# Kernel tuning notes

Measured on AMD Instinct MI355X. Metric: run time of the kernel, lower is better.

The kernel has to match this reference:

```python
import jax, jax.numpy as jnp
import numpy as np

N, C, H, W = 4, 256, 64, 64
K, G, PAD, STRIDE, DIL = 3, 8, 1, 1, 1
GC = C // G      # channels per group
P = K * K        # sampling points per group
HIN, WIN = H + 2 * PAD, W + 2 * PAD
BN_EPS = 1e-5
LN_EPS = 1e-5


def setup_inputs():
    key = jax.random.key(0)
    ks = jax.random.split(key, 8)
    f32 = jnp.float32
    return {
        "x": jax.random.normal(ks[0], (N, C, H, W), dtype=f32),
        "w_in": jax.random.normal(ks[1], (C, C), dtype=f32) * 0.05,
        "b_in": jnp.zeros((C,), f32),
        "w_dw": jax.random.normal(ks[2], (C, 1, K, K), dtype=f32) * 0.1,
        "b_dw": jnp.zeros((C,), f32),
        "ln_g": jnp.ones((C,), f32), "ln_b": jnp.zeros((C,), f32),
        "w_off": jax.random.normal(ks[3], (C, G * P * 2), dtype=f32) * 0.01,
        "b_off": jax.random.normal(ks[4], (G * P * 2,), dtype=f32) * 0.01,
        "w_mask": jax.random.normal(ks[5], (C, G * P), dtype=f32) * 0.01,
        "b_mask": jnp.zeros((G * P,), f32),
        "w_out": jax.random.normal(ks[6], (C, C), dtype=f32) * 0.05,
        "b_out": jnp.zeros((C,), f32),
        "bn_g": jnp.ones((C,), f32), "bn_b": jnp.zeros((C,), f32),
        "bn_mean": jnp.zeros((C,), f32), "bn_var": jnp.ones((C,), f32),
    }


def _bilinear(img, grid):
    # img: (B, Cc, Hh, Ww); grid: (B, S, P, 2) normalized to [-1,1],
    # matches F.grid_sample(mode='bilinear', padding_mode='zeros', align_corners=False)
    B, Cc, Hh, Ww = img.shape
    gx = (grid[..., 0] + 1.0) * 0.5 * Ww - 0.5
    gy = (grid[..., 1] + 1.0) * 0.5 * Hh - 0.5
    x0 = jnp.floor(gx)
    y0 = jnp.floor(gy)
    wx = gx - x0
    wy = gy - y0
    flat = img.reshape(B, Cc, Hh * Ww)

    def tap(xi, yi, wgt):
        valid = (xi >= 0) & (xi <= Ww - 1) & (yi >= 0) & (yi <= Hh - 1)
        idx = (jnp.clip(yi, 0, Hh - 1) * Ww + jnp.clip(xi, 0, Ww - 1)).astype(jnp.int32)
        v = jax.vmap(lambda im, ix: im[:, ix])(flat, idx)   # (B, Cc, S, P)
        return v * (wgt * valid.astype(img.dtype))[:, None]

    return (tap(x0, y0, (1 - wx) * (1 - wy)) + tap(x0 + 1, y0, wx * (1 - wy))
            + tap(x0, y0 + 1, (1 - wx) * wy) + tap(x0 + 1, y0 + 1, wx * wy))


def _forward(x, w_in, b_in, w_dw, b_dw, ln_g, ln_b, w_off, b_off,
             w_mask, b_mask, w_out, b_out, bn_g, bn_b, bn_mean, bn_var):
    xl = jnp.transpose(x, (0, 2, 3, 1))                      # (N,H,W,C) channels-last
    x_proj = xl @ w_in + b_in                                # input_proj
    # depthwise conv + LayerNorm + GELU feature branch for offset/mask prediction
    dw = jax.lax.conv_general_dilated(
        x, w_dw, (1, 1), ((PAD, PAD), (PAD, PAD)),
        feature_group_count=C, dimension_numbers=("NCHW", "OIHW", "NCHW"))
    dw = jnp.transpose(dw + b_dw[None, :, None, None], (0, 2, 3, 1))
    mu = dw.mean(-1, keepdims=True)
    var = ((dw - mu) ** 2).mean(-1, keepdims=True)
    dw = (dw - mu) * jax.lax.rsqrt(var + LN_EPS) * ln_g + ln_b
    x1 = jax.nn.gelu(dw, approximate=False)
    offset = x1 @ w_off + b_off                              # (N,H,W,G*P*2)
    mask = jax.nn.softmax((x1 @ w_mask + b_mask).reshape(N, H, W, G, P), axis=-1)
    # reference points + dilation kernel grid, normalized to padded input, (x,y) order
    ry = ((DIL * (K - 1)) // 2 + 0.5 + jnp.arange(H, dtype=x.dtype) * STRIDE) / HIN
    rx = ((DIL * (K - 1)) // 2 + 0.5 + jnp.arange(W, dtype=x.dtype) * STRIDE) / WIN
    ref = jnp.stack(jnp.broadcast_arrays(rx[None, :], ry[:, None]), axis=-1)  # (H,W,2)
    px = (jnp.arange(K, dtype=x.dtype) * DIL - (DIL * (K - 1)) // 2) / WIN
    py = (jnp.arange(K, dtype=x.dtype) * DIL - (DIL * (K - 1)) // 2) / HIN
    gx, gy = jnp.meshgrid(px, py, indexing="ij")             # kw-major flattening as in DCNv3
    kgrid = jnp.stack([gx, gy], -1).reshape(P, 2)
    norm = jnp.array([WIN, HIN], dtype=x.dtype)
    loc = (ref[None, :, :, None, None, :] + kgrid[None, None, None, None, :, :]
           + offset.reshape(N, H, W, G, P, 2) / norm)        # (N,H,W,G,P,2), offset_scale=1
    sgrid = 2.0 * loc - 1.0
    # group-split padded value tensor and deformable sampling
    xp = jnp.pad(x_proj, ((0, 0), (PAD, PAD), (PAD, PAD), (0, 0)))
    img = jnp.transpose(xp, (0, 3, 1, 2)).reshape(N * G, GC, HIN, WIN)
    sg = jnp.transpose(sgrid.reshape(N, H * W, G, P, 2), (0, 2, 1, 3, 4)).reshape(N * G, H * W, P, 2)
    sampled = _bilinear(img, sg)                             # (N*G, GC, H*W, P)
    m = jnp.transpose(mask.reshape(N, H * W, G, P), (0, 2, 1, 3)).reshape(N * G, 1, H * W, P)
    agg = (sampled * m).sum(-1)                              # (N*G, GC, H*W)
    y = jnp.transpose(agg.reshape(N, C, H * W), (0, 2, 1)).reshape(N, H, W, C)
    y = y @ w_out + b_out                                    # output_proj
    y = jnp.transpose(y, (0, 3, 1, 2))                       # back to NCHW
    y = (y - bn_mean[None, :, None, None]) * jax.lax.rsqrt(bn_var + BN_EPS)[None, :, None, None]
    y = y * bn_g[None, :, None, None] + bn_b[None, :, None, None]
    return y * jax.nn.sigmoid(y)                             # SiLU (Conv.default_act)


def reference(x, w_in, b_in, w_dw, b_dw, ln_g, ln_b, w_off, b_off,
              w_mask, b_mask, w_out, b_out, bn_g, bn_b, bn_mean, bn_var):
    return _forward(x, w_in, b_in, w_dw, b_dw, ln_g, ln_b, w_off, b_off,
                    w_mask, b_mask, w_out, b_out, bn_g, bn_b, bn_mean, bn_var)
```

## Files before the change

### kernel.cpp

```cpp
#include <hip/hip_runtime.h>
#include <math.h>

#define NB   4
#define CCH  256
#define HH   64
#define WW   64
#define GG   8
#define GCH  32
#define PP   9
#define HIN  66
#define WIN  66
#define HWSZ 4096
#define NPIX 16384

#define X16_ELEMS (NPIX*CCH)
#define XP_ELEMS  (NB*HIN*WIN*CCH)
#define X1_ELEMS  (NPIX*CCH)
#define AGG_ELEMS (NPIX*CCH)
#define WIN16_ELEMS (CCH*CCH)
#define WOUT16_ELEMS (CCH*CCH)
#define WOM16_ELEMS (CCH*216)
#define OFF_ELEMS (NPIX*144)
#define MSK_ELEMS (NPIX*72)

typedef __attribute__((ext_vector_type(8))) short bf16x8;
typedef __attribute__((ext_vector_type(4))) float f32x4;

__device__ __forceinline__ unsigned short f2bf(float f) {
    unsigned int u = __float_as_uint(f);
    unsigned int r = (u + 0x7FFFu + ((u >> 16) & 1u)) >> 16;
    return (unsigned short)r;
}
__device__ __forceinline__ float bf2f(unsigned short s) {
    return __uint_as_float(((unsigned int)s) << 16);
}

#define AK 40

__global__ __launch_bounds__(256) void k_prep(
    const float* __restrict__ x, const float* __restrict__ w_in,
    const float* __restrict__ w_off, const float* __restrict__ w_mask,
    const float* __restrict__ w_out, unsigned short* __restrict__ x16,
    unsigned short* __restrict__ w_in16, unsigned short* __restrict__ wom16,
    unsigned short* __restrict__ w_out16, unsigned short* __restrict__ xp)
{
    const int b = blockIdx.x;
    const int tid = threadIdx.x;
    if (b < 2048) {
        size_t i0 = (size_t)b * 2048 + tid * 4;
#pragma unroll
        for (int h = 0; h < 2; h++) {
            float4 v = *(const float4*)&x[i0 + h * 1024];
            ushort4 o;
            o.x = f2bf(v.x); o.y = f2bf(v.y); o.z = f2bf(v.z); o.w = f2bf(v.w);
            *(ushort4*)&x16[i0 + h * 1024] = o;
        }
    } else if (b < 2096) {
        int gtid = (b - 2048) * 256 + tid;
        for (int i = gtid; i < 186368; i += 12288) {
            if (i < 65536) {
                w_in16[i] = f2bf(w_in[i]);
            } else if (i < 131072) {
                int j = i - 65536;
                w_out16[j] = f2bf(w_out[j]);
            } else {
                int j = i - 131072;
                int r = j / 216, c = j - r * 216;
                float v = (c < 144) ? w_off[r * 144 + c] : w_mask[r * 72 + c - 144];
                wom16[j] = f2bf(v);
            }
        }
    } else {
        int idx = (b - 2096) * 256 + tid;
        int seg = idx >> 6, ln = idx & 63;
        int n = seg / 260, rp = seg % 260;
        int h, w;
        if (rp < 66)       { h = 0;        w = rp; }
        else if (rp < 132) { h = 65;       w = rp - 66; }
        else if (rp < 196) { h = rp - 131; w = 0; }
        else               { h = rp - 195; w = 65; }
        uint2 z = make_uint2(0u, 0u);
        *(uint2*)&xp[(((size_t)n * HIN + h) * WIN + w) * CCH + ln * 4] = z;
    }
}

__global__ __launch_bounds__(256) void k_gemm_in(
    const unsigned short* __restrict__ x16, const unsigned short* __restrict__ w16,
    const float* __restrict__ b_in, unsigned short* __restrict__ xp)
{
    __shared__ short As[128 * AK];
    __shared__ short Ws[64 * AK];

    const int m0  = blockIdx.x * 128;
    const int co0 = blockIdx.y * 64;
    const int tid = threadIdx.x;
    const int n   = m0 >> 12;
    const int hw0 = m0 & 4095;

    const int wave = tid >> 6;
    const int lane = tid & 63;
    const int r16  = lane & 15;
    const int quad = lane >> 4;
    const int mw   = wave * 32;

    const unsigned short* xa = x16 + (size_t)n * CCH * HWSZ + hw0;

    f32x4 acc[2][4];
#pragma unroll
    for (int i = 0; i < 2; i++)
#pragma unroll
        for (int j = 0; j < 4; j++) acc[i][j] = (f32x4){0.f, 0.f, 0.f, 0.f};

    for (int k0 = 0; k0 < CCH; k0 += 32) {
#pragma unroll
        for (int l = 0; l < 4; l++) {
            int idx = tid + l * 256;
            int m = idx & 127, kph = idx >> 7;
            unsigned int u0 = xa[(size_t)(k0 + 4 * kph + 0) * HWSZ + m];
            unsigned int u1 = xa[(size_t)(k0 + 4 * kph + 1) * HWSZ + m];
            unsigned int u2 = xa[(size_t)(k0 + 4 * kph + 2) * HWSZ + m];
            unsigned int u3 = xa[(size_t)(k0 + 4 * kph + 3) * HWSZ + m];
            uint2 pk = make_uint2(u0 | (u1 << 16), u2 | (u3 << 16));
            *(uint2*)&As[m * AK + kph * 4] = pk;
        }
#pragma unroll
        for (int l = 0; l < 2; l++) {
            int idx = tid + l * 256;
            int nn = idx & 63, kph = idx >> 6;
            unsigned int u0 = w16[(size_t)(k0 + 4 * kph + 0) * CCH + co0 + nn];
            unsigned int u1 = w16[(size_t)(k0 + 4 * kph + 1) * CCH + co0 + nn];
            unsigned int u2 = w16[(size_t)(k0 + 4 * kph + 2) * CCH + co0 + nn];
            unsigned int u3 = w16[(size_t)(k0 + 4 * kph + 3) * CCH + co0 + nn];
            uint2 pk = make_uint2(u0 | (u1 << 16), u2 | (u3 << 16));
            *(uint2*)&Ws[nn * AK + kph * 4] = pk;
        }
        __syncthreads();

        bf16x8 a0 = *(const bf16x8*)&As[(mw + r16) * AK + quad * 8];
        bf16x8 a1 = *(const bf16x8*)&As[(mw + 16 + r16) * AK + quad * 8];
#pragma unroll
        for (int nt = 0; nt < 4; nt++) {
            bf16x8 bfr = *(const bf16x8*)&Ws[(nt * 16 + r16) * AK + quad * 8];
            acc[0][nt] = __builtin_amdgcn_mfma_f32_16x16x32_bf16(a0, bfr, acc[0][nt], 0, 0, 0);
            acc[1][nt] = __builtin_amdgcn_mfma_f32_16x16x32_bf16(a1, bfr, acc[1][nt], 0, 0, 0);
        }
        __syncthreads();
    }

#pragma unroll
    for (int nt = 0; nt < 4; nt++) {
        int co = co0 + nt * 16 + r16;
        float bias = b_in[co];
#pragma unroll
        for (int mt = 0; mt < 2; mt++) {
            int mbase = mw + mt * 16 + quad * 4;
#pragma unroll
            for (int r = 0; r < 4; r++) {
                int hw = hw0 + mbase + r;
                int h = hw >> 6, w = hw & 63;
                xp[(((size_t)n * HIN + (h + 1)) * WIN + (w + 1)) * CCH + co] =
                    f2bf(acc[mt][nt][r] + bias);
            }
        }
    }
}

#define SDW_STRIDE 258
__global__ __launch_bounds__(512) void k_dw_ln_gelu(
    const unsigned short* __restrict__ x16, const float* __restrict__ w_dw,
    const float* __restrict__ b_dw, const float* __restrict__ ln_g,
    const float* __restrict__ ln_b, unsigned short* __restrict__ x1)
{
    __shared__ unsigned short sdw[64 * SDW_STRIDE];
    __shared__ float r1s[8][64];
    __shared__ float r2s[8][64];
    __shared__ float mu_s[64];
    __shared__ float rs_s[64];

    const int h = blockIdx.x;
    const int n = blockIdx.y;
    const int tid = threadIdx.x;
    const int wave = tid >> 6;
    const int lane = tid & 63;

    const unsigned short* xn = x16 + (size_t)n * CCH * HWSZ;
    const bool h0ok = (h > 0);
    const bool h2ok = (h < HH - 1);

    float s1 = 0.f, s2 = 0.f;

#pragma unroll 4
    for (int it = 0; it < 32; it++) {
        const int c = it * 8 + wave;
        const unsigned short* xc = xn + (size_t)c * HWSZ + h * WW + lane;
        float v0 = h0ok ? bf2f(xc[-WW]) : 0.f;
        float v1 = bf2f(xc[0]);
        float v2 = h2ok ? bf2f(xc[WW]) : 0.f;

        const float* wk = w_dw + c * 9;
        float acc = b_dw[c];

        float l0 = __shfl_up(v0, 1);  if (lane == 0)  l0 = 0.f;
        float r0 = __shfl_down(v0, 1); if (lane == 63) r0 = 0.f;
        acc += wk[0] * l0 + wk[1] * v0 + wk[2] * r0;

        float l1 = __shfl_up(v1, 1);  if (lane == 0)  l1 = 0.f;
        float r1 = __shfl_down(v1, 1); if (lane == 63) r1 = 0.f;
        acc += wk[3] * l1 + wk[4] * v1 + wk[5] * r1;

        float l2 = __shfl_up(v2, 1);  if (lane == 0)  l2 = 0.f;
        float r2 = __shfl_down(v2, 1); if (lane == 63) r2 = 0.f;
        acc += wk[6] * l2 + wk[7] * v2 + wk[8] * r2;

        s1 += acc;
        s2 += acc * acc;
        sdw[lane * SDW_STRIDE + c] = f2bf(acc);
    }

    r1s[wave][lane] = s1;
    r2s[wave][lane] = s2;
    __syncthreads();

    if (tid < 64) {
        float a1 = 0.f, a2 = 0.f;
#pragma unroll
        for (int q = 0; q < 8; q++) { a1 += r1s[q][tid]; a2 += r2s[q][tid]; }
        float mu = a1 * (1.0f / 256.0f);
        float var = a2 * (1.0f / 256.0f) - mu * mu;
        mu_s[tid] = mu;
        rs_s[tid] = rsqrtf(var + 1e-5f);
    }
    __syncthreads();

    const int c0 = (tid & 63) * 4;
    const int wq = tid >> 6;
    float g4[4], b4[4];
#pragma unroll
    for (int i = 0; i < 4; i++) { g4[i] = ln_g[c0 + i]; b4[i] = ln_b[c0 + i]; }

    unsigned short* x1p = x1 + (((size_t)n * HH + h) * WW) * CCH + c0;
#pragma unroll
    for (int pass = 0; pass < 8; pass++) {
        int w = wq + pass * 8;
        float mu = mu_s[w], rs = rs_s[w];
        const unsigned short* row = &sdw[w * SDW_STRIDE + c0];
        unsigned short tmp[4];
#pragma unroll
        for (int i = 0; i < 4; i++) {
            float v = (bf2f(row[i]) - mu) * rs * g4[i] + b4[i];
            tmp[i] = f2bf(0.5f * v * (1.0f + erff(v * 0.70710678118654752f)));
        }
        ushort4 o; o.x = tmp[0]; o.y = tmp[1]; o.z = tmp[2]; o.w = tmp[3];
        *(ushort4*)&x1p[(size_t)w * CCH] = o;
    }
}

__global__ __launch_bounds__(256) void k_gemm_offmask(
    const unsigned short* __restrict__ x1, const unsigned short* __restrict__ wom16,
    const float* __restrict__ b_off, const float* __restrict__ b_mask,
    float* __restrict__ off, float* __restrict__ msk)
{
    __shared__ short As[128 * AK];
    __shared__ short Ws[64 * AK];

    const int m0  = blockIdx.x * 128;
    const int co0 = blockIdx.y * 64;
    const int tid = threadIdx.x;

    const int wave = tid >> 6;
    const int lane = tid & 63;
    const int r16  = lane & 15;
    const int quad = lane >> 4;
    const int mw   = wave * 32;

    f32x4 acc[2][4];
#pragma unroll
    for (int i = 0; i < 2; i++)
#pragma unroll
        for (int j = 0; j < 4; j++) acc[i][j] = (f32x4){0.f, 0.f, 0.f, 0.f};

    for (int k0 = 0; k0 < CCH; k0 += 32) {
#pragma unroll
        for (int l = 0; l < 2; l++) {
            int idx = tid + l * 256;
            int m = idx >> 2, kq = idx & 3;
            uint4 v = *(const uint4*)&x1[(size_t)(m0 + m) * CCH + k0 + kq * 8];
            *(uint4*)&As[m * AK + kq * 8] = v;
        }
#pragma unroll
        for (int l = 0; l < 2; l++) {
            int idx = tid + l * 256;
            int nn = idx & 63, kph = idx >> 6;
            int col = co0 + nn;
            unsigned int u0 = 0, u1 = 0, u2 = 0, u3 = 0;
            if (col < 216) {
                u0 = wom16[(size_t)(k0 + 4 * kph + 0) * 216 + col];
                u1 = wom16[(size_t)(k0 + 4 * kph + 1) * 216 + col];
                u2 = wom16[(size_t)(k0 + 4 * kph + 2) * 216 + col];
                u3 = wom16[(size_t)(k0 + 4 * kph + 3) * 216 + col];
            }
            uint2 pk = make_uint2(u0 | (u1 << 16), u2 | (u3 << 16));
            *(uint2*)&Ws[nn * AK + kph * 4] = pk;
        }
        __syncthreads();

        bf16x8 a0 = *(const bf16x8*)&As[(mw + r16) * AK + quad * 8];
        bf16x8 a1 = *(const bf16x8*)&As[(mw + 16 + r16) * AK + quad * 8];
#pragma unroll
        for (int nt = 0; nt < 4; nt++) {
            bf16x8 bfr = *(const bf16x8*)&Ws[(nt * 16 + r16) * AK + quad * 8];
            acc[0][nt] = __builtin_amdgcn_mfma_f32_16x16x32_bf16(a0, bfr, acc[0][nt], 0, 0, 0);
            acc[1][nt] = __builtin_amdgcn_mfma_f32_16x16x32_bf16(a1, bfr, acc[1][nt], 0, 0, 0);
        }
        __syncthreads();
    }

#pragma unroll
    for (int nt = 0; nt < 4; nt++) {
        int col = co0 + nt * 16 + r16;
        if (col >= 216) continue;
        float bias = (col < 144) ? b_off[col] : b_mask[col - 144];
#pragma unroll
        for (int mt = 0; mt < 2; mt++) {
            int mbase = m0 + mw + mt * 16 + quad * 4;
#pragma unroll
            for (int r = 0; r < 4; r++) {
                int p = mbase + r;
                float v = acc[mt][nt][r] + bias;
                if (col < 144) off[(size_t)p * 144 + col] = v;
                else           msk[(size_t)p * 72 + col - 144] = v;
            }
        }
    }
}

__device__ __forceinline__ void acc8_tap(float* a, uint4 vv, float wgt) {
    a[0] += wgt * __uint_as_float(vv.x << 16);
    a[1] += wgt * __uint_as_float(vv.x & 0xffff0000u);
    a[2] += wgt * __uint_as_float(vv.y << 16);
    a[3] += wgt * __uint_as_float(vv.y & 0xffff0000u);
    a[4] += wgt * __uint_as_float(vv.z << 16);
    a[5] += wgt * __uint_as_float(vv.z & 0xffff0000u);
    a[6] += wgt * __uint_as_float(vv.w << 16);
    a[7] += wgt * __uint_as_float(vv.w & 0xffff0000u);
}

__global__ __launch_bounds__(256) void k_sample_agg(
    const unsigned short* __restrict__ xp, const float* __restrict__ off,
    const float* __restrict__ msk, unsigned short* __restrict__ agg)
{
    __shared__ float  sm[576];
    __shared__ int2   tco[576];
    __shared__ float4 twt[576];

    const int tid = threadIdx.x;
    const int s0 = blockIdx.x * 8;

    if (tid < 64) {
        const int pix = tid >> 3, g = tid & 7;
        const float* mskp = msk + (size_t)(s0 + pix) * 72 + g * 9;
        float e[9];
        float mx = -1e30f;
#pragma unroll
        for (int p = 0; p < PP; p++) { e[p] = mskp[p]; mx = fmaxf(mx, e[p]); }
        float sum = 0.f;
#pragma unroll
        for (int p = 0; p < PP; p++) { e[p] = __expf(e[p] - mx); sum += e[p]; }
        float rs = 1.0f / sum;
#pragma unroll
        for (int p = 0; p < PP; p++) sm[tid * 9 + p] = e[p] * rs;
    }
    __syncthreads();

    for (int idx = tid; idx < 576; idx += 256) {
        int pix = idx / 72;
        int rem = idx - pix * 72;
        int g = rem / 9;
        int p = rem - g * 9;
        int s = s0 + pix;
        int hw = s & 4095;
        int h = hw >> 6, w = hw & 63;
        const float* offp = off + (size_t)s * 144 + g * 18 + p * 2;
        float ox = offp[0], oy = offp[1];
        int i = p / 3, j = p - i * 3;
        float fx = (float)(w + i) + ox;
        float fy = (float)(h + j) + oy;
        float x0f = floorf(fx), y0f = floorf(fy);
        int x0 = (int)x0f, y0 = (int)y0f;
        float wx = fx - x0f, wy = fy - y0f;
        float m = sm[idx];
        float w00 = (1.f - wx) * (1.f - wy) * m;
        float w10 = wx * (1.f - wy) * m;
        float w01 = (1.f - wx) * wy * m;
        float w11 = wx * wy * m;
        int x1c = x0 + 1, y1c = y0 + 1;
        if (!((x0  >= 0) && (x0  < WIN))) { w00 = 0.f; w01 = 0.f; }
        if (!((x1c >= 0) && (x1c < WIN))) { w10 = 0.f; w11 = 0.f; }
        if (!((y0  >= 0) && (y0  < HIN))) { w00 = 0.f; w10 = 0.f; }
        if (!((y1c >= 0) && (y1c < HIN))) { w01 = 0.f; w11 = 0.f; }
        int cx0 = min(max(x0, 0), WIN - 1), cx1 = min(max(x1c, 0), WIN - 1);
        int cy0 = min(max(y0, 0), HIN - 1), cy1 = min(max(y1c, 0), HIN - 1);
        tco[idx] = make_int2(cx0 | (cx1 << 16), cy0 | (cy1 << 16));
        twt[idx] = make_float4(w00, w10, w01, w11);
    }
    __syncthreads();

    const int pix = tid >> 5;
    const int l5 = tid & 31;
    const int g = l5 >> 2, c8 = l5 & 3;
    const int s = s0 + pix;
    const int n = s >> 12;
    const unsigned short* base = xp + (size_t)n * HIN * WIN * CCH + g * GCH + c8 * 8;
    const int tbase = pix * 72 + g * 9;

    float a[8];
#pragma unroll
    for (int i = 0; i < 8; i++) a[i] = 0.f;

#pragma unroll
    for (int p = 0; p < PP; p++) {
        int2 cc = tco[tbase + p];
        float4 wt = twt[tbase + p];
        int cx0 = cc.x & 0xFFFF, cx1 = cc.x >> 16;
        int cy0 = cc.y & 0xFFFF, cy1 = cc.y >> 16;
        const unsigned short* r0 = base + (size_t)(cy0 * WIN) * CCH;
        const unsigned short* r1 = base + (size_t)(cy1 * WIN) * CCH;
        uint4 v00 = *(const uint4*)&r0[(size_t)cx0 * CCH];
        uint4 v10 = *(const uint4*)&r0[(size_t)cx1 * CCH];
        uint4 v01 = *(const uint4*)&r1[(size_t)cx0 * CCH];
        uint4 v11 = *(const uint4*)&r1[(size_t)cx1 * CCH];
        acc8_tap(a, v00, wt.x);
        acc8_tap(a, v10, wt.y);
        acc8_tap(a, v01, wt.z);
        acc8_tap(a, v11, wt.w);
    }

    uint4 o;
    o.x = (unsigned int)f2bf(a[0]) | ((unsigned int)f2bf(a[1]) << 16);
    o.y = (unsigned int)f2bf(a[2]) | ((unsigned int)f2bf(a[3]) << 16);
    o.z = (unsigned int)f2bf(a[4]) | ((unsigned int)f2bf(a[5]) << 16);
    o.w = (unsigned int)f2bf(a[6]) | ((unsigned int)f2bf(a[7]) << 16);
    *(uint4*)&agg[(size_t)s * CCH + g * GCH + c8 * 8] = o;
}

__global__ __launch_bounds__(256) void k_gemm_out(
    const unsigned short* __restrict__ agg, const unsigned short* __restrict__ w16,
    const float* __restrict__ b_out, const float* __restrict__ bn_g,
    const float* __restrict__ bn_b, const float* __restrict__ bn_mean,
    const float* __restrict__ bn_var, float* __restrict__ out)
{
    __shared__ short As[128 * AK];
    __shared__ short Ws[64 * AK];

    const int m0  = blockIdx.x * 128;
    const int co0 = blockIdx.y * 64;
    const int tid = threadIdx.x;
    const int n   = m0 >> 12;
    const int hw0 = m0 & 4095;

    const int wave = tid >> 6;
    const int lane = tid & 63;
    const int r16  = lane & 15;
    const int quad = lane >> 4;
    const int mw   = wave * 32;

    f32x4 acc[2][4];
#pragma unroll
    for (int i = 0; i < 2; i++)
#pragma unroll
        for (int j = 0; j < 4; j++) acc[i][j] = (f32x4){0.f, 0.f, 0.f, 0.f};

    for (int k0 = 0; k0 < CCH; k0 += 32) {
#pragma unroll
        for (int l = 0; l < 2; l++) {
            int idx = tid + l * 256;
            int m = idx >> 2, kq = idx & 3;
            uint4 v = *(const uint4*)&agg[(size_t)(m0 + m) * CCH + k0 + kq * 8];
            *(uint4*)&As[m * AK + kq * 8] = v;
        }
#pragma unroll
        for (int l = 0; l < 2; l++) {
            int idx = tid + l * 256;
            int nn = idx & 63, kph = idx >> 6;
            unsigned int u0 = w16[(size_t)(k0 + 4 * kph + 0) * CCH + co0 + nn];
            unsigned int u1 = w16[(size_t)(k0 + 4 * kph + 1) * CCH + co0 + nn];
            unsigned int u2 = w16[(size_t)(k0 + 4 * kph + 2) * CCH + co0 + nn];
            unsigned int u3 = w16[(size_t)(k0 + 4 * kph + 3) * CCH + co0 + nn];
            uint2 pk = make_uint2(u0 | (u1 << 16), u2 | (u3 << 16));
            *(uint2*)&Ws[nn * AK + kph * 4] = pk;
        }
        __syncthreads();

        bf16x8 a0 = *(const bf16x8*)&As[(mw + r16) * AK + quad * 8];
        bf16x8 a1 = *(const bf16x8*)&As[(mw + 16 + r16) * AK + quad * 8];
#pragma unroll
        for (int nt = 0; nt < 4; nt++) {
            bf16x8 bfr = *(const bf16x8*)&Ws[(nt * 16 + r16) * AK + quad * 8];
            acc[0][nt] = __builtin_amdgcn_mfma_f32_16x16x32_bf16(a0, bfr, acc[0][nt], 0, 0, 0);
            acc[1][nt] = __builtin_amdgcn_mfma_f32_16x16x32_bf16(a1, bfr, acc[1][nt], 0, 0, 0);
        }
        __syncthreads();
    }

#pragma unroll
    for (int nt = 0; nt < 4; nt++) {
        int co = co0 + nt * 16 + r16;
        float mean = bn_mean[co];
        float rstd = rsqrtf(bn_var[co] + 1e-5f);
        float gg = bn_g[co], bb = bn_b[co], bo = b_out[co];
#pragma unroll
        for (int mt = 0; mt < 2; mt++) {
            int hwb = hw0 + mw + mt * 16 + quad * 4;
            float tmp[4];
#pragma unroll
            for (int r = 0; r < 4; r++) {
                float y = acc[mt][nt][r] + bo;
                float yh = (y - mean) * rstd * gg + bb;
                tmp[r] = yh / (1.0f + __expf(-yh));
            }
            float4 v = make_float4(tmp[0], tmp[1], tmp[2], tmp[3]);
            *(float4*)&out[((size_t)n * CCH + co) * HWSZ + hwb] = v;
        }
    }
}

extern "C" void kernel_launch(void* const* d_in, const int* in_sizes, int n_in,
                              void* d_out, int out_size, void* d_ws, size_t ws_size,
                              hipStream_t stream)
{
    const float* x       = (const float*)d_in[0];
    const float* w_in    = (const float*)d_in[1];
    const float* b_in    = (const float*)d_in[2];
    const float* w_dw    = (const float*)d_in[3];
    const float* b_dw    = (const float*)d_in[4];
    const float* ln_g    = (const float*)d_in[5];
    const float* ln_b    = (const float*)d_in[6];
    const float* w_off   = (const float*)d_in[7];
    const float* b_off   = (const float*)d_in[8];
    const float* w_mask  = (const float*)d_in[9];
    const float* b_mask  = (const float*)d_in[10];
    const float* w_out   = (const float*)d_in[11];
    const float* b_out   = (const float*)d_in[12];
    const float* bn_g    = (const float*)d_in[13];
    const float* bn_b    = (const float*)d_in[14];
    const float* bn_mean = (const float*)d_in[15];
    const float* bn_var  = (const float*)d_in[16];
    float* out = (float*)d_out;

    unsigned short* x16    = (unsigned short*)d_ws;
    unsigned short* xp     = x16 + X16_ELEMS;
    unsigned short* x1     = xp + XP_ELEMS;
    unsigned short* agg    = x1 + X1_ELEMS;
    unsigned short* w_in16 = agg + AGG_ELEMS;
    unsigned short* w_out16= w_in16 + WIN16_ELEMS;
    unsigned short* wom16  = w_out16 + WOUT16_ELEMS;
    float* off = (float*)(wom16 + WOM16_ELEMS);
    float* msk = off + OFF_ELEMS;

    k_prep<<<dim3(2356), 256, 0, stream>>>(x, w_in, w_off, w_mask, w_out,
                                           x16, w_in16, wom16, w_out16, xp);
    k_gemm_in<<<dim3(128, 4), 256, 0, stream>>>(x16, w_in16, b_in, xp);
    k_dw_ln_gelu<<<dim3(64, 4), 512, 0, stream>>>(x16, w_dw, b_dw, ln_g, ln_b, x1);
    k_gemm_offmask<<<dim3(128, 4), 256, 0, stream>>>(x1, wom16, b_off, b_mask, off, msk);
    k_sample_agg<<<dim3(2048), 256, 0, stream>>>(xp, off, msk, agg);
    k_gemm_out<<<dim3(128, 4), 256, 0, stream>>>(agg, w_out16, b_out, bn_g, bn_b, bn_mean, bn_var, out);
}
```

Measured before the change: 198.6 us.

## Fuse prep with depthwise-LN-GELU, merge input and offset GEMMs, drop LDS staging

The bf16 conversion of x now happens inside the depthwise/LayerNorm/GELU kernel, which reads fp32 x directly and also writes an NHWC bf16 copy of x. That kernel is merged with the weight-transpose and padding work into one launch. The input projection and the offset/mask projection GEMMs now share one launch with 1024 blocks. All GEMMs load A fragments and transposed weight fragments straight from global memory, with no shared-memory tiles or barriers. This cuts the launch count from six to four and removes a strided NCHW gather and the LDS round trips. The cost is more redundant global/L2 traffic for the weight fragments, and a dw kernel with more shared memory and only 256 compute blocks.

```diff
diff --git a/kernel.cpp b/kernel.cpp
--- a/kernel.cpp
+++ b/kernel.cpp
@@ -13,15 +13,15 @@
 #define HWSZ 4096
 #define NPIX 16384
 
-#define X16_ELEMS (NPIX*CCH)
-#define XP_ELEMS  (NB*HIN*WIN*CCH)
-#define X1_ELEMS  (NPIX*CCH)
-#define AGG_ELEMS (NPIX*CCH)
-#define WIN16_ELEMS (CCH*CCH)
-#define WOUT16_ELEMS (CCH*CCH)
-#define WOM16_ELEMS (CCH*216)
-#define OFF_ELEMS (NPIX*144)
-#define MSK_ELEMS (NPIX*72)
+#define X16_ELEMS  (NPIX*CCH)
+#define XP_ELEMS   (NB*HIN*WIN*CCH)
+#define X1_ELEMS   (NPIX*CCH)
+#define AGG_ELEMS  (NPIX*CCH)
+#define WINT_ELEMS (CCH*CCH)
+#define WOUTT_ELEMS (CCH*CCH)
+#define WOMT_ELEMS (216*CCH)
+#define OFF_ELEMS  (NPIX*144)
+#define MSK_ELEMS  (NPIX*72)
 
 typedef __attribute__((ext_vector_type(8))) short bf16x8;
 typedef __attribute__((ext_vector_type(4))) float f32x4;
@@ -35,300 +35,238 @@
     return __uint_as_float(((unsigned int)s) << 16);
 }
 
-#define AK 40
-
-__global__ __launch_bounds__(256) void k_prep(
-    const float* __restrict__ x, const float* __restrict__ w_in,
+#define SDW_STRIDE 258
+
+__global__ __launch_bounds__(512) void k_dw_prep(
+    const float* __restrict__ x, const float* __restrict__ w_dw,
+    const float* __restrict__ b_dw, const float* __restrict__ ln_g,
+    const float* __restrict__ ln_b, const float* __restrict__ w_in,
     const float* __restrict__ w_off, const float* __restrict__ w_mask,
-    const float* __restrict__ w_out, unsigned short* __restrict__ x16,
-    unsigned short* __restrict__ w_in16, unsigned short* __restrict__ wom16,
-    unsigned short* __restrict__ w_out16, unsigned short* __restrict__ xp)
+    const float* __restrict__ w_out, unsigned short* __restrict__ x1,
+    unsigned short* __restrict__ x16, unsigned short* __restrict__ win_t,
+    unsigned short* __restrict__ womt, unsigned short* __restrict__ wout_t,
+    unsigned short* __restrict__ xp)
 {
     const int b = blockIdx.x;
     const int tid = threadIdx.x;
-    if (b < 2048) {
-        size_t i0 = (size_t)b * 2048 + tid * 4;
-#pragma unroll
-        for (int h = 0; h < 2; h++) {
-            float4 v = *(const float4*)&x[i0 + h * 1024];
-            ushort4 o;
-            o.x = f2bf(v.x); o.y = f2bf(v.y); o.z = f2bf(v.z); o.w = f2bf(v.w);
-            *(ushort4*)&x16[i0 + h * 1024] = o;
-        }
-    } else if (b < 2096) {
-        int gtid = (b - 2048) * 256 + tid;
-        for (int i = gtid; i < 186368; i += 12288) {
+
+    if (b >= 256) {
+        const int gtid = (b - 256) * 512 + tid;
+        const int STRIDE = 68 * 512;
+        for (int i = gtid; i < 252928; i += STRIDE) {
             if (i < 65536) {
-                w_in16[i] = f2bf(w_in[i]);
+                int n = i & 255, k = i >> 8;
+                win_t[n * 256 + k] = f2bf(w_in[i]);
             } else if (i < 131072) {
                 int j = i - 65536;
-                w_out16[j] = f2bf(w_out[j]);
+                int n = j & 255, k = j >> 8;
+                wout_t[n * 256 + k] = f2bf(w_out[j]);
+            } else if (i < 186368) {
+                int j = i - 131072;
+                int k = j / 216, col = j - k * 216;
+                float v = (col < 144) ? w_off[k * 144 + col]
+                                      : w_mask[k * 72 + col - 144];
+                womt[col * 256 + k] = f2bf(v);
             } else {
-                int j = i - 131072;
-                int r = j / 216, c = j - r * 216;
-                float v = (c < 144) ? w_off[r * 144 + c] : w_mask[r * 72 + c - 144];
-                wom16[j] = f2bf(v);
-            }
-        }
-    } else {
-        int idx = (b - 2096) * 256 + tid;
-        int seg = idx >> 6, ln = idx & 63;
-        int n = seg / 260, rp = seg % 260;
-        int h, w;
-        if (rp < 66)       { h = 0;        w = rp; }
-        else if (rp < 132) { h = 65;       w = rp - 66; }
-        else if (rp < 196) { h = rp - 131; w = 0; }
-        else               { h = rp - 195; w = 65; }
-        uint2 z = make_uint2(0u, 0u);
-        *(uint2*)&xp[(((size_t)n * HIN + h) * WIN + w) * CCH + ln * 4] = z;
-    }
-}
-
-__global__ __launch_bounds__(256) void k_gemm_in(
-    const unsigned short* __restrict__ x16, const unsigned short* __restrict__ w16,
-    const float* __restrict__ b_in, unsigned short* __restrict__ xp)
+                int r = i - 186368;
+                int seg = r >> 6, ln = r & 63;
+                int n = seg / 260, rp = seg % 260;
+                int h, w;
+                if (rp < 66)       { h = 0;        w = rp; }
+                else if (rp < 132) { h = 65;       w = rp - 66; }
+                else if (rp < 196) { h = rp - 131; w = 0; }
+                else               { h = rp - 195; w = 65; }
+                uint2 z = make_uint2(0u, 0u);
+                *(uint2*)&xp[(((size_t)n * HIN + h) * WIN + w) * CCH + ln * 4] = z;
+            }
+        }
+        return;
+    }
+
+    __shared__ unsigned short sdw[64 * SDW_STRIDE];
+    __shared__ unsigned short sxr[64 * SDW_STRIDE];
+    __shared__ float r1s[8][64];
+    __shared__ float r2s[8][64];
+    __shared__ float mu_s[64];
+    __shared__ float rs_s[64];
+
+    const int h = b & 63;
+    const int n = b >> 6;
+    const int wave = tid >> 6;
+    const int lane = tid & 63;
+
+    const float* xn = x + (size_t)n * CCH * HWSZ;
+    const bool h0ok = (h > 0);
+    const bool h2ok = (h < HH - 1);
+
+    float s1 = 0.f, s2 = 0.f;
+
+#pragma unroll 4
+    for (int it = 0; it < 32; it++) {
+        const int c = it * 8 + wave;
+        const float* xc = xn + (size_t)c * HWSZ + h * WW + lane;
+        float v0 = h0ok ? xc[-WW] : 0.f;
+        float v1 = xc[0];
+        float v2 = h2ok ? xc[WW] : 0.f;
+
+        const float* wk = w_dw + c * 9;
+        float acc = b_dw[c];
+
+        float l0 = __shfl_up(v0, 1);   if (lane == 0)  l0 = 0.f;
+        float r0 = __shfl_down(v0, 1); if (lane == 63) r0 = 0.f;
+        acc += wk[0] * l0 + wk[1] * v0 + wk[2] * r0;
+
+        float l1 = __shfl_up(v1, 1);   if (lane == 0)  l1 = 0.f;
+        float r1 = __shfl_down(v1, 1); if (lane == 63) r1 = 0.f;
+        acc += wk[3] * l1 + wk[4] * v1 + wk[5] * r1;
+
+        float l2 = __shfl_up(v2, 1);   if (lane == 0)  l2 = 0.f;
+        float r2 = __shfl_down(v2, 1); if (lane == 63) r2 = 0.f;
+        acc += wk[6] * l2 + wk[7] * v2 + wk[8] * r2;
+
+        s1 += acc;
+        s2 += acc * acc;
+        sdw[lane * SDW_STRIDE + c] = f2bf(acc);
+        sxr[lane * SDW_STRIDE + c] = f2bf(v1);
+    }
+
+    r1s[wave][lane] = s1;
+    r2s[wave][lane] = s2;
+    __syncthreads();
+
+    if (tid < 64) {
+        float a1 = 0.f, a2 = 0.f;
+#pragma unroll
+        for (int q = 0; q < 8; q++) { a1 += r1s[q][tid]; a2 += r2s[q][tid]; }
+        float mu = a1 * (1.0f / 256.0f);
+        float var = a2 * (1.0f / 256.0f) - mu * mu;
+        mu_s[tid] = mu;
+        rs_s[tid] = rsqrtf(var + 1e-5f);
+    }
+    __syncthreads();
+
+    const int c0 = (tid & 63) * 4;
+    const int wq = tid >> 6;
+    float g4[4], b4[4];
+#pragma unroll
+    for (int i = 0; i < 4; i++) { g4[i] = ln_g[c0 + i]; b4[i] = ln_b[c0 + i]; }
+
+    unsigned short* x1p  = x1  + (((size_t)n * HH + h) * WW) * CCH + c0;
+    unsigned short* x16p = x16 + (((size_t)n * HH + h) * WW) * CCH + c0;
+#pragma unroll
+    for (int pass = 0; pass < 8; pass++) {
+        int w = wq + pass * 8;
+        float mu = mu_s[w], rs = rs_s[w];
+        const unsigned short* row  = &sdw[w * SDW_STRIDE + c0];
+        const unsigned short* rowx = &sxr[w * SDW_STRIDE + c0];
+        unsigned short tmp[4];
+#pragma unroll
+        for (int i = 0; i < 4; i++) {
+            float v = (bf2f(row[i]) - mu) * rs * g4[i] + b4[i];
+            tmp[i] = f2bf(0.5f * v * (1.0f + erff(v * 0.70710678118654752f)));
+        }
+        ushort4 o; o.x = tmp[0]; o.y = tmp[1]; o.z = tmp[2]; o.w = tmp[3];
+        *(ushort4*)&x1p[(size_t)w * CCH] = o;
+        ushort4 xo; xo.x = rowx[0]; xo.y = rowx[1]; xo.z = rowx[2]; xo.w = rowx[3];
+        *(ushort4*)&x16p[(size_t)w * CCH] = xo;
+    }
+}
+
+__global__ __launch_bounds__(256) void k_proj(
+    const unsigned short* __restrict__ x16, const unsigned short* __restrict__ win_t,
+    const float* __restrict__ b_in, unsigned short* __restrict__ xp,
+    const unsigned short* __restrict__ x1, const unsigned short* __restrict__ womt,
+    const float* __restrict__ b_off, const float* __restrict__ b_mask,
+    float* __restrict__ off, float* __restrict__ msk)
 {
-    __shared__ short As[128 * AK];
-    __shared__ short Ws[64 * AK];
-
-    const int m0  = blockIdx.x * 128;
-    const int co0 = blockIdx.y * 64;
+    const int b = blockIdx.x;
     const int tid = threadIdx.x;
-    const int n   = m0 >> 12;
-    const int hw0 = m0 & 4095;
-
     const int wave = tid >> 6;
     const int lane = tid & 63;
     const int r16  = lane & 15;
     const int quad = lane >> 4;
     const int mw   = wave * 32;
 
-    const unsigned short* xa = x16 + (size_t)n * CCH * HWSZ + hw0;
-
     f32x4 acc[2][4];
 #pragma unroll
     for (int i = 0; i < 2; i++)
 #pragma unroll
         for (int j = 0; j < 4; j++) acc[i][j] = (f32x4){0.f, 0.f, 0.f, 0.f};
 
-    for (int k0 = 0; k0 < CCH; k0 += 32) {
-#pragma unroll
-        for (int l = 0; l < 4; l++) {
-            int idx = tid + l * 256;
-            int m = idx & 127, kph = idx >> 7;
-            unsigned int u0 = xa[(size_t)(k0 + 4 * kph + 0) * HWSZ + m];
-            unsigned int u1 = xa[(size_t)(k0 + 4 * kph + 1) * HWSZ + m];
-            unsigned int u2 = xa[(size_t)(k0 + 4 * kph + 2) * HWSZ + m];
-            unsigned int u3 = xa[(size_t)(k0 + 4 * kph + 3) * HWSZ + m];
-            uint2 pk = make_uint2(u0 | (u1 << 16), u2 | (u3 << 16));
-            *(uint2*)&As[m * AK + kph * 4] = pk;
-        }
-#pragma unroll
-        for (int l = 0; l < 2; l++) {
-            int idx = tid + l * 256;
-            int nn = idx & 63, kph = idx >> 6;
-            unsigned int u0 = w16[(size_t)(k0 + 4 * kph + 0) * CCH + co0 + nn];
-            unsigned int u1 = w16[(size_t)(k0 + 4 * kph + 1) * CCH + co0 + nn];
-            unsigned int u2 = w16[(size_t)(k0 + 4 * kph + 2) * CCH + co0 + nn];
-            unsigned int u3 = w16[(size_t)(k0 + 4 * kph + 3) * CCH + co0 + nn];
-            uint2 pk = make_uint2(u0 | (u1 << 16), u2 | (u3 << 16));
-            *(uint2*)&Ws[nn * AK + kph * 4] = pk;
-        }
-        __syncthreads();
-
-        bf16x8 a0 = *(const bf16x8*)&As[(mw + r16) * AK + quad * 8];
-        bf16x8 a1 = *(const bf16x8*)&As[(mw + 16 + r16) * AK + quad * 8];
+    if (b < 512) {
+        const int m0  = (b & 127) * 128;
+        const int co0 = (b >> 7) * 64;
+        const int n   = m0 >> 12;
+        const int hw0 = m0 & 4095;
+
+        const unsigned short* a0p = x16 + (size_t)(m0 + mw + r16) * CCH + quad * 8;
+        const unsigned short* a1p = a0p + 16 * CCH;
+
+#pragma unroll
+        for (int k0 = 0; k0 < CCH; k0 += 32) {
+            bf16x8 a0 = *(const bf16x8*)&a0p[k0];
+            bf16x8 a1 = *(const bf16x8*)&a1p[k0];
+#pragma unroll
+            for (int nt = 0; nt < 4; nt++) {
+                bf16x8 bfr = *(const bf16x8*)&win_t[(size_t)(co0 + nt * 16 + r16) * CCH + k0 + quad * 8];
+                acc[0][nt] = __builtin_amdgcn_mfma_f32_16x16x32_bf16(a0, bfr, acc[0][nt], 0, 0, 0);
+                acc[1][nt] = __builtin_amdgcn_mfma_f32_16x16x32_bf16(a1, bfr, acc[1][nt], 0, 0, 0);
+            }
+        }
+
 #pragma unroll
         for (int nt = 0; nt < 4; nt++) {
-            bf16x8 bfr = *(const bf16x8*)&Ws[(nt * 16 + r16) * AK + quad * 8];
-            acc[0][nt] = __builtin_amdgcn_mfma_f32_16x16x32_bf16(a0, bfr, acc[0][nt], 0, 0, 0);
-            acc[1][nt] = __builtin_amdgcn_mfma_f32_16x16x32_bf16(a1, bfr, acc[1][nt], 0, 0, 0);
-        }
-        __syncthreads();
-    }
-
-#pragma unroll
-    for (int nt = 0; nt < 4; nt++) {
-        int co = co0 + nt * 16 + r16;
-        float bias = b_in[co];
-#pragma unroll
-        for (int mt = 0; mt < 2; mt++) {
-            int mbase = mw + mt * 16 + quad * 4;
-#pragma unroll
-            for (int r = 0; r < 4; r++) {
-                int hw = hw0 + mbase + r;
-                int h = hw >> 6, w = hw & 63;
-                xp[(((size_t)n * HIN + (h + 1)) * WIN + (w + 1)) * CCH + co] =
-                    f2bf(acc[mt][nt][r] + bias);
-            }
-        }
-    }
-}
-
-#define SDW_STRIDE 258
-__global__ __launch_bounds__(512) void k_dw_ln_gelu(
-    const unsigned short* __restrict__ x16, const float* __restrict__ w_dw,
-    const float* __restrict__ b_dw, const float* __restrict__ ln_g,
-    const float* __restrict__ ln_b, unsigned short* __restrict__ x1)
-{
-    __shared__ unsigned short sdw[64 * SDW_STRIDE];
-    __shared__ float r1s[8][64];
-    __shared__ float r2s[8][64];
-    __shared__ float mu_s[64];
-    __shared__ float rs_s[64];
-
-    const int h = blockIdx.x;
-    const int n = blockIdx.y;
-    const int tid = threadIdx.x;
-    const int wave = tid >> 6;
-    const int lane = tid & 63;
-
-    const unsigned short* xn = x16 + (size_t)n * CCH * HWSZ;
-    const bool h0ok = (h > 0);
-    const bool h2ok = (h < HH - 1);
-
-    float s1 = 0.f, s2 = 0.f;
-
-#pragma unroll 4
-    for (int it = 0; it < 32; it++) {
-        const int c = it * 8 + wave;
-        const unsigned short* xc = xn + (size_t)c * HWSZ + h * WW + lane;
-        float v0 = h0ok ? bf2f(xc[-WW]) : 0.f;
-        float v1 = bf2f(xc[0]);
-        float v2 = h2ok ? bf2f(xc[WW]) : 0.f;
-
-        const float* wk = w_dw + c * 9;
-        float acc = b_dw[c];
-
-        float l0 = __shfl_up(v0, 1);  if (lane == 0)  l0 = 0.f;
-        float r0 = __shfl_down(v0, 1); if (lane == 63) r0 = 0.f;
-        acc += wk[0] * l0 + wk[1] * v0 + wk[2] * r0;
-
-        float l1 = __shfl_up(v1, 1);  if (lane == 0)  l1 = 0.f;
-        float r1 = __shfl_down(v1, 1); if (lane == 63) r1 = 0.f;
-        acc += wk[3] * l1 + wk[4] * v1 + wk[5] * r1;
-
-        float l2 = __shfl_up(v2, 1);  if (lane == 0)  l2 = 0.f;
-        float r2 = __shfl_down(v2, 1); if (lane == 63) r2 = 0.f;
-        acc += wk[6] * l2 + wk[7] * v2 + wk[8] * r2;
-
-        s1 += acc;
-        s2 += acc * acc;
-        sdw[lane * SDW_STRIDE + c] = f2bf(acc);
-    }
-
-    r1s[wave][lane] = s1;
-    r2s[wave][lane] = s2;
-    __syncthreads();
-
-    if (tid < 64) {
-        float a1 = 0.f, a2 = 0.f;
-#pragma unroll
-        for (int q = 0; q < 8; q++) { a1 += r1s[q][tid]; a2 += r2s[q][tid]; }
-        float mu = a1 * (1.0f / 256.0f);
-        float var = a2 * (1.0f / 256.0f) - mu * mu;
-        mu_s[tid] = mu;
-        rs_s[tid] = rsqrtf(var + 1e-5f);
-    }
-    __syncthreads();
-
-    const int c0 = (tid & 63) * 4;
-    const int wq = tid >> 6;
-    float g4[4], b4[4];
-#pragma unroll
-    for (int i = 0; i < 4; i++) { g4[i] = ln_g[c0 + i]; b4[i] = ln_b[c0 + i]; }
-
-    unsigned short* x1p = x1 + (((size_t)n * HH + h) * WW) * CCH + c0;
-#pragma unroll
-    for (int pass = 0; pass < 8; pass++) {
-        int w = wq + pass * 8;
-        float mu = mu_s[w], rs = rs_s[w];
-        const unsigned short* row = &sdw[w * SDW_STRIDE + c0];
-        unsigned short tmp[4];
-#pragma unroll
-        for (int i = 0; i < 4; i++) {
-            float v = (bf2f(row[i]) - mu) * rs * g4[i] + b4[i];
-            tmp[i] = f2bf(0.5f * v * (1.0f + erff(v * 0.70710678118654752f)));
-        }
-        ushort4 o; o.x = tmp[0]; o.y = tmp[1]; o.z = tmp[2]; o.w = tmp[3];
-        *(ushort4*)&x1p[(size_t)w * CCH] = o;
-    }
-}
-
-__global__ __launch_bounds__(256) void k_gemm_offmask(
-    const unsigned short* __restrict__ x1, const unsigned short* __restrict__ wom16,
-    const float* __restrict__ b_off, const float* __restrict__ b_mask,
-    float* __restrict__ off, float* __restrict__ msk)
-{
-    __shared__ short As[128 * AK];
-    __shared__ short Ws[64 * AK];
-
-    const int m0  = blockIdx.x * 128;
-    const int co0 = blockIdx.y * 64;
-    const int tid = threadIdx.x;
-
-    const int wave = tid >> 6;
-    const int lane = tid & 63;
-    const int r16  = lane & 15;
-    const int quad = lane >> 4;
-    const int mw   = wave * 32;
-
-    f32x4 acc[2][4];
-#pragma unroll
-    for (int i = 0; i < 2; i++)
-#pragma unroll
-        for (int j = 0; j < 4; j++) acc[i][j] = (f32x4){0.f, 0.f, 0.f, 0.f};
-
-    for (int k0 = 0; k0 < CCH; k0 += 32) {
-#pragma unroll
-        for (int l = 0; l < 2; l++) {
-            int idx = tid + l * 256;
-            int m = idx >> 2, kq = idx & 3;
-            uint4 v = *(const uint4*)&x1[(size_t)(m0 + m) * CCH + k0 + kq * 8];
-            *(uint4*)&As[m * AK + kq * 8] = v;
-        }
-#pragma unroll
-        for (int l = 0; l < 2; l++) {
-            int idx = tid + l * 256;
-            int nn = idx & 63, kph = idx >> 6;
-            int col = co0 + nn;
-            unsigned int u0 = 0, u1 = 0, u2 = 0, u3 = 0;
-            if (col < 216) {
-                u0 = wom16[(size_t)(k0 + 4 * kph + 0) * 216 + col];
-                u1 = wom16[(size_t)(k0 + 4 * kph + 1) * 216 + col];
-                u2 = wom16[(size_t)(k0 + 4 * kph + 2) * 216 + col];
-                u3 = wom16[(size_t)(k0 + 4 * kph + 3) * 216 + col];
-            }
-            uint2 pk = make_uint2(u0 | (u1 << 16), u2 | (u3 << 16));
-            *(uint2*)&Ws[nn * AK + kph * 4] = pk;
-        }
-        __syncthreads();
-
-        bf16x8 a0 = *(const bf16x8*)&As[(mw + r16) * AK + quad * 8];
-        bf16x8 a1 = *(const bf16x8*)&As[(mw + 16 + r16) * AK + quad * 8];
+            int co = co0 + nt * 16 + r16;
+            float bias = b_in[co];
+#pragma unroll
+            for (int mt = 0; mt < 2; mt++) {
+                int mbase = mw + mt * 16 + quad * 4;
+#pragma unroll
+                for (int r = 0; r < 4; r++) {
+                    int hw = hw0 + mbase + r;
+                    int h = hw >> 6, w = hw & 63;
+                    xp[(((size_t)n * HIN + (h + 1)) * WIN + (w + 1)) * CCH + co] =
+                        f2bf(acc[mt][nt][r] + bias);
+                }
+            }
+        }
+    } else {
+        const int b2 = b - 512;
+        const int m0  = (b2 & 127) * 128;
+        const int co0 = (b2 >> 7) * 64;
+
+        const unsigned short* a0p = x1 + (size_t)(m0 + mw + r16) * CCH + quad * 8;
+        const unsigned short* a1p = a0p + 16 * CCH;
+
+#pragma unroll
+        for (int k0 = 0; k0 < CCH; k0 += 32) {
+            bf16x8 a0 = *(const bf16x8*)&a0p[k0];
+            bf16x8 a1 = *(const bf16x8*)&a1p[k0];
+#pragma unroll
+            for (int nt = 0; nt < 4; nt++) {
+                int col = co0 + nt * 16 + r16;
+                int colc = (col < 216) ? col : 215;
+                bf16x8 bfr = *(const bf16x8*)&womt[(size_t)colc * CCH + k0 + quad * 8];
+                acc[0][nt] = __builtin_amdgcn_mfma_f32_16x16x32_bf16(a0, bfr, acc[0][nt], 0, 0, 0);
+                acc[1][nt] = __builtin_amdgcn_mfma_f32_16x16x32_bf16(a1, bfr, acc[1][nt], 0, 0, 0);
+            }
+        }
+
 #pragma unroll
         for (int nt = 0; nt < 4; nt++) {
-            bf16x8 bfr = *(const bf16x8*)&Ws[(nt * 16 + r16) * AK + quad * 8];
-            acc[0][nt] = __builtin_amdgcn_mfma_f32_16x16x32_bf16(a0, bfr, acc[0][nt], 0, 0, 0);
-            acc[1][nt] = __builtin_amdgcn_mfma_f32_16x16x32_bf16(a1, bfr, acc[1][nt], 0, 0, 0);
-        }
-        __syncthreads();
-    }
-
-#pragma unroll
-    for (int nt = 0; nt < 4; nt++) {
-        int col = co0 + nt * 16 + r16;
-        if (col >= 216) continue;
-        float bias = (col < 144) ? b_off[col] : b_mask[col - 144];
-#pragma unroll
-        for (int mt = 0; mt < 2; mt++) {
-            int mbase = m0 + mw + mt * 16 + quad * 4;
-#pragma unroll
-            for (int r = 0; r < 4; r++) {
-                int p = mbase + r;
-                float v = acc[mt][nt][r] + bias;
-                if (col < 144) off[(size_t)p * 144 + col] = v;
-                else           msk[(size_t)p * 72 + col - 144] = v;
+            int col = co0 + nt * 16 + r16;
+            if (col >= 216) continue;
+            float bias = (col < 144) ? b_off[col] : b_mask[col - 144];
+#pragma unroll
+            for (int mt = 0; mt < 2; mt++) {
+                int mbase = m0 + mw + mt * 16 + quad * 4;
+#pragma unroll
+                for (int r = 0; r < 4; r++) {
+                    int p = mbase + r;
+                    float v = acc[mt][nt][r] + bias;
+                    if (col < 144) off[(size_t)p * 144 + col] = v;
+                    else           msk[(size_t)p * 72 + col - 144] = v;
+                }
             }
         }
     }
@@ -444,14 +382,11 @@
 }
 
 __global__ __launch_bounds__(256) void k_gemm_out(
-    const unsigned short* __restrict__ agg, const unsigned short* __restrict__ w16,
+    const unsigned short* __restrict__ agg, const unsigned short* __restrict__ wout_t,
     const float* __restrict__ b_out, const float* __restrict__ bn_g,
     const float* __restrict__ bn_b, const float* __restrict__ bn_mean,
     const float* __restrict__ bn_var, float* __restrict__ out)
 {
-    __shared__ short As[128 * AK];
-    __shared__ short Ws[64 * AK];
-
     const int m0  = blockIdx.x * 128;
     const int co0 = blockIdx.y * 64;
     const int tid = threadIdx.x;
@@ -470,36 +405,19 @@
 #pragma unroll
         for (int j = 0; j < 4; j++) acc[i][j] = (f32x4){0.f, 0.f, 0.f, 0.f};
 
+    const unsigned short* a0p = agg + (size_t)(m0 + mw + r16) * CCH + quad * 8;
+    const unsigned short* a1p = a0p + 16 * CCH;
+
+#pragma unroll
     for (int k0 = 0; k0 < CCH; k0 += 32) {
-#pragma unroll
-        for (int l = 0; l < 2; l++) {
-            int idx = tid + l * 256;
-            int m = idx >> 2, kq = idx & 3;
-            uint4 v = *(const uint4*)&agg[(size_t)(m0 + m) * CCH + k0 + kq * 8];
-            *(uint4*)&As[m * AK + kq * 8] = v;
-        }
-#pragma unroll
-        for (int l = 0; l < 2; l++) {
-            int idx = tid + l * 256;
-            int nn = idx & 63, kph = idx >> 6;
-            unsigned int u0 = w16[(size_t)(k0 + 4 * kph + 0) * CCH + co0 + nn];
-            unsigned int u1 = w16[(size_t)(k0 + 4 * kph + 1) * CCH + co0 + nn];
-            unsigned int u2 = w16[(size_t)(k0 + 4 * kph + 2) * CCH + co0 + nn];
-            unsigned int u3 = w16[(size_t)(k0 + 4 * kph + 3) * CCH + co0 + nn];
-            uint2 pk = make_uint2(u0 | (u1 << 16), u2 | (u3 << 16));
-            *(uint2*)&Ws[nn * AK + kph * 4] = pk;
-        }
-        __syncthreads();
-
-        bf16x8 a0 = *(const bf16x8*)&As[(mw + r16) * AK + quad * 8];
-        bf16x8 a1 = *(const bf16x8*)&As[(mw + 16 + r16) * AK + quad * 8];
+        bf16x8 a0 = *(const bf16x8*)&a0p[k0];
+        bf16x8 a1 = *(const bf16x8*)&a1p[k0];
 #pragma unroll
         for (int nt = 0; nt < 4; nt++) {
-            bf16x8 bfr = *(const bf16x8*)&Ws[(nt * 16 + r16) * AK + quad * 8];
+            bf16x8 bfr = *(const bf16x8*)&wout_t[(size_t)(co0 + nt * 16 + r16) * CCH + k0 + quad * 8];
             acc[0][nt] = __builtin_amdgcn_mfma_f32_16x16x32_bf16(a0, bfr, acc[0][nt], 0, 0, 0);
             acc[1][nt] = __builtin_amdgcn_mfma_f32_16x16x32_bf16(a1, bfr, acc[1][nt], 0, 0, 0);
         }
-        __syncthreads();
     }
 
 #pragma unroll
@@ -547,21 +465,21 @@
     const float* bn_var  = (const float*)d_in[16];
     float* out = (float*)d_out;
 
-    unsigned short* x16    = (unsigned short*)d_ws;
-    unsigned short* xp     = x16 + X16_ELEMS;
-    unsigned short* x1     = xp + XP_ELEMS;
+    unsigned short* xp     = (unsigned short*)d_ws;
+    unsigned short* x16    = xp + XP_ELEMS;
+    unsigned short* x1     = x16 + X16_ELEMS;
     unsigned short* agg    = x1 + X1_ELEMS;
-    unsigned short* w_in16 = agg + AGG_ELEMS;
-    unsigned short* w_out16= w_in16 + WIN16_ELEMS;
-    unsigned short* wom16  = w_out16 + WOUT16_ELEMS;
-    float* off = (float*)(wom16 + WOM16_ELEMS);
+    unsigned short* win_t  = agg + AGG_ELEMS;
+    unsigned short* wout_t = win_t + WINT_ELEMS;
+    unsigned short* womt   = wout_t + WOUTT_ELEMS;
+    float* off = (float*)(womt + WOMT_ELEMS);
     float* msk = off + OFF_ELEMS;
 
-    k_prep<<<dim3(2356), 256, 0, stream>>>(x, w_in, w_off, w_mask, w_out,
-                                           x16, w_in16, wom16, w_out16, xp);
-    k_gemm_in<<<dim3(128, 4), 256, 0, stream>>>(x16, w_in16, b_in, xp);
-    k_dw_ln_gelu<<<dim3(64, 4), 512, 0, stream>>>(x16, w_dw, b_dw, ln_g, ln_b, x1);
-    k_gemm_offmask<<<dim3(128, 4), 256, 0, stream>>>(x1, wom16, b_off, b_mask, off, msk);
+    k_dw_prep<<<dim3(324), 512, 0, stream>>>(x, w_dw, b_dw, ln_g, ln_b,
+                                             w_in, w_off, w_mask, w_out,
+                                             x1, x16, win_t, womt, wout_t, xp);
+    k_proj<<<dim3(1024), 256, 0, stream>>>(x16, win_t, b_in, xp,
+                                           x1, womt, b_off, b_mask, off, msk);
     k_sample_agg<<<dim3(2048), 256, 0, stream>>>(xp, off, msk, agg);
-    k_gemm_out<<<dim3(128, 4), 256, 0, stream>>>(agg, w_out16, b_out, bn_g, bn_b, bn_mean, bn_var, out);
-}
+    k_gemm_out<<<dim3(128, 4), 256, 0, stream>>>(agg, wout_t, b_out, bn_g, bn_b, bn_mean, bn_var, out);
+}
```

Result: faster. 179.2 us, median of 2 (-9.8%).
